# Optimization experiments

Measured on AMD Instinct MI355X. Metric: run time of the kernel, lower is better.

The kernel has to match this reference:

```python
import jax, jax.numpy as jnp
import numpy as np
import math

B, C, H, W = 4, 256, 64, 64
HID = 32  # max(C//8, 32)

def setup_inputs() -> dict:
    key = jax.random.key(0)
    ks = jax.random.split(key, 7)
    x = jax.random.normal(ks[0], (B, C, H, W), dtype=jnp.float32)
    # 1x1 conv weights stored as [out, in]
    w_ce1 = jax.random.normal(ks[1], (HID, C), dtype=jnp.float32) * math.sqrt(2.0 / HID)
    w_ce2 = jax.random.normal(ks[2], (1, HID), dtype=jnp.float32) * math.sqrt(2.0)
    xav = math.sqrt(6.0 / (C + C))
    wq = jax.random.uniform(ks[3], (C, C), jnp.float32, -xav, xav)
    wk = jax.random.uniform(ks[4], (C, C), jnp.float32, -xav, xav)
    wv = jax.random.uniform(ks[5], (C, C), jnp.float32, -xav, xav)
    wproj = jax.random.uniform(ks[6], (C, C), jnp.float32, -xav, xav)
    return {"x": x, "w_ce1": w_ce1, "w_ce2": w_ce2, "wq": wq, "wk": wk, "wv": wv, "wproj": wproj}

def reference(x, w_ce1, w_ce2, wq, wk, wv, wproj):
    b, c, h, w = x.shape
    n = h * w
    # complexity gate: global avg+max pool -> 1x1 convs -> sigmoid, shape [B,1,1,1]
    feat = jnp.mean(x, axis=(2, 3)) + jnp.max(x, axis=(2, 3))       # [B,C]
    hid = jax.nn.silu(jnp.einsum('oc,bc->bo', w_ce1, feat))          # [B,HID]
    complexity = jax.nn.sigmoid(jnp.einsum('oh,bh->bo', w_ce2, hid)) # [B,1]
    complexity = complexity[:, :, None, None]                        # [B,1,1,1]
    # qkv via 1x1 convs, flattened to tokens
    xf = x.reshape(b, c, n)                                          # [B,C,N]
    q = jnp.einsum('oc,bcn->bno', wq, xf)                            # [B,N,C]
    k = jnp.einsum('oc,bcn->bon', wk, xf)                            # [B,C,N]
    v = jnp.einsum('oc,bcn->bno', wv, xf)                            # [B,N,C]
    attn = jax.nn.softmax(jnp.einsum('bnc,bcm->bnm', q, k) * (1.0 / math.sqrt(c)), axis=-1)
    x_attn = jnp.einsum('bnm,bmc->bnc', attn, v)                     # [B,N,C]
    x_attn = x_attn.transpose(0, 2, 1).reshape(b, c, h, w)           # [B,C,H,W]
    proj = jnp.einsum('oc,bchw->bohw', wproj, x_attn)
    return x + proj * complexity
```

## Files before the change

### kernel.cpp

```cpp
#include <hip/hip_runtime.h>
#include <hip/hip_bf16.h>

#define B_ 4
#define C_ 256
#define N_ 4096
#define BN_ (B_*N_)

typedef float f32x4 __attribute__((ext_vector_type(4)));
typedef short bf16x8 __attribute__((ext_vector_type(8)));
typedef short short4v __attribute__((ext_vector_type(4)));

static __device__ __forceinline__ short f2bf(float f){
  unsigned u = __builtin_bit_cast(unsigned, f);
  u += 0x7FFFu + ((u >> 16) & 1u);
  return (short)(u >> 16);
}
static __device__ __forceinline__ float bf2f(short s){
  unsigned u = ((unsigned)(unsigned short)s) << 16;
  return __builtin_bit_cast(float, u);
}
static __device__ __forceinline__ void gload_lds16(const void* g, void* l){
  __builtin_amdgcn_global_load_lds((const __attribute__((address_space(1))) unsigned*)g,
                                   (__attribute__((address_space(3))) unsigned*)l, 16, 0, 0);
}

__global__ __launch_bounds__(256) void k_feat(const float* __restrict__ x, float* __restrict__ feat){
  int row = blockIdx.x;
  const f32x4* p = (const f32x4*)(x + (size_t)row * N_);
  float s = 0.f, mx = -1e30f;
  for (int i = threadIdx.x; i < N_/4; i += 256){
    f32x4 v = p[i];
    s += v.x + v.y + v.z + v.w;
    mx = fmaxf(mx, fmaxf(fmaxf(v.x, v.y), fmaxf(v.z, v.w)));
  }
  __shared__ float ss[256];
  __shared__ float sm[256];
  int t = threadIdx.x;
  ss[t] = s; sm[t] = mx;
  __syncthreads();
  for (int off = 128; off > 0; off >>= 1){
    if (t < off){ ss[t] += ss[t+off]; sm[t] = fmaxf(sm[t], sm[t+off]); }
    __syncthreads();
  }
  if (t == 0) feat[row] = ss[0] * (1.f/(float)N_) + sm[0];
}

__global__ __launch_bounds__(64) void k_cplx(const float* __restrict__ feat, const float* __restrict__ w1,
    const float* __restrict__ w2, float* __restrict__ cplx){
  int b = blockIdx.x, l = threadIdx.x;
  float contrib = 0.f;
  if (l < 32){
    const float* wr = w1 + l*C_;
    const float* f = feat + b*C_;
    float d = 0.f;
    for (int c = 0; c < C_; c++) d += wr[c]*f[c];
    float sg = 1.f/(1.f + expf(-d));
    contrib = (d*sg)*w2[l];
  }
  #pragma unroll
  for (int off = 1; off < 64; off <<= 1) contrib += __shfl_xor(contrib, off);
  if (l == 0) cplx[b] = 1.f/(1.f + expf(-contrib));
}

__global__ __launch_bounds__(256) void k_wcvt(const float* __restrict__ a, const float* __restrict__ b,
    const float* __restrict__ c, const float* __restrict__ d,
    short* __restrict__ oa, short* __restrict__ ob2, short* __restrict__ oc, short* __restrict__ od){
  int m = blockIdx.x >> 6;
  int off = (blockIdx.x & 63)*1024 + threadIdx.x*4;
  const float* src = (m==0)?a:(m==1)?b:(m==2)?c:d;
  short* dst = (m==0)?oa:(m==1)?ob2:(m==2)?oc:od;
  f32x4 v = *(const f32x4*)(src + off);
  short4v s;
  #pragma unroll
  for (int j = 0; j < 4; j++) s[j] = f2bf(v[j]);
  *(short4v*)(dst + off) = s;
}

__global__ __launch_bounds__(256) void k_qkv(const float* __restrict__ x,
    const short* __restrict__ wqb, const short* __restrict__ wkb, const short* __restrict__ wvb,
    short* __restrict__ Q, short* __restrict__ K, short* __restrict__ Vt){
  int b = blockIdx.z, o0 = blockIdx.y*64, n0 = blockIdx.x*64;
  int tid = threadIdx.x, w = tid>>6, l = tid&63, lq = l&15, lg = l>>4;
  const float* xb = x + (size_t)b*C_*N_;
  int nrow = n0 + w*16 + lq;
  f32x4 zero = {0.f,0.f,0.f,0.f};
  f32x4 acc[3][4];
  #pragma unroll
  for (int m = 0; m < 3; m++)
    #pragma unroll
    for (int s = 0; s < 4; s++) acc[m][s] = zero;

  for (int kk = 0; kk < 8; ++kk){
    int c0 = kk*32 + lg*8;
    bf16x8 a;
    #pragma unroll
    for (int j = 0; j < 8; j++) a[j] = f2bf(xb[(size_t)(c0+j)*N_ + nrow]);
    #pragma unroll
    for (int s = 0; s < 4; s++){
      int base = (o0 + s*16 + lq)*C_ + c0;
      bf16x8 aq = *(const bf16x8*)(wqb + base);
      bf16x8 ak = *(const bf16x8*)(wkb + base);
      bf16x8 av = *(const bf16x8*)(wvb + base);
      acc[0][s] = __builtin_amdgcn_mfma_f32_16x16x32_bf16(a, aq, acc[0][s], 0, 0, 0);
      acc[1][s] = __builtin_amdgcn_mfma_f32_16x16x32_bf16(a, ak, acc[1][s], 0, 0, 0);
      acc[2][s] = __builtin_amdgcn_mfma_f32_16x16x32_bf16(a, av, acc[2][s], 0, 0, 0);
    }
  }
  #pragma unroll
  for (int s = 0; s < 4; s++)
    #pragma unroll
    for (int r = 0; r < 4; r++){
      int n = n0 + w*16 + lg*4 + r;
      int o = o0 + s*16 + lq;
      size_t idx = ((size_t)b*N_ + n)*C_ + o;
      Q[idx] = f2bf(acc[0][s][r] * 0.0625f);
      K[idx] = f2bf(acc[1][s][r]);
    }
  __shared__ short lv[64][72];
  #pragma unroll
  for (int s = 0; s < 4; s++)
    #pragma unroll
    for (int r = 0; r < 4; r++)
      lv[s*16 + lq][w*16 + lg*4 + r] = f2bf(acc[2][s][r]);
  __syncthreads();
  #pragma unroll
  for (int i = 0; i < 16; i++){
    int orow = i*4 + (tid>>6);
    int ncol = tid & 63;
    Vt[((size_t)b*C_ + o0 + orow)*N_ + n0 + ncol] = lv[orow][ncol];
  }
}

__global__ __launch_bounds__(512) void k_attn(const short* __restrict__ Q, const short* __restrict__ K,
    const short* __restrict__ Vt, short* __restrict__ Op, float* __restrict__ Mp, float* __restrict__ Lp){
  extern __shared__ short smem[];
  short* Ks = smem;
  short* Vs = smem + 32768;

  int bid = blockIdx.x;
  int xcd = bid & 7;
  int b = xcd >> 1;
  int half = xcd & 1;
  int n0 = (bid >> 3) * 128;
  int kv0 = half * 2048;
  int tid = threadIdx.x, w = tid>>6, l = tid&63, lq = l&15, lg = l>>4;
  const short* Qb = Q + (size_t)b*N_*C_;
  const short* Kb = K + (size_t)b*N_*C_;
  const short* Vb = Vt + (size_t)b*C_*N_;
  short* lp = smem + 65536 + w*(16*72);

  int krow0 = w*8 + (l>>5);
  int kchunk0 = l&31;
  int vrow0 = w*32 + (l>>3);
  int vchunk = (l&7) ^ ((l>>3)&7);

  bf16x8 qf[8];
  {
    const short* qrow = Qb + (size_t)(n0 + w*16 + lq)*C_ + lg*8;
    #pragma unroll
    for (int kk = 0; kk < 8; kk++) qf[kk] = *(const bf16x8*)(qrow + kk*32);
  }
  f32x4 zero = {0.f,0.f,0.f,0.f};
  f32x4 oacc[16];
  #pragma unroll
  for (int c = 0; c < 16; c++) oacc[c] = zero;
  float mrow[4], lsum[4];
  #pragma unroll
  for (int r = 0; r < 4; r++){ mrow[r] = -1e30f; lsum[r] = 0.f; }

  int swz = lq & 7;

  auto stage = [&](int buf, int m0){
    short* kd = Ks + buf*16384 + w*2048;
    short* vd = Vs + buf*16384 + w*2048;
    #pragma unroll
    for (int i = 0; i < 4; i++){
      int row = krow0 + i*2;
      int chunk = kchunk0 ^ (row & 7);
      gload_lds16(Kb + (size_t)(m0 + row)*C_ + chunk*8, kd + i*512);
    }
    #pragma unroll
    for (int i = 0; i < 4; i++){
      int row = vrow0 + i*8;
      gload_lds16(Vb + (size_t)row*N_ + m0 + vchunk*8, vd + i*512);
    }
  };

  stage(0, kv0);
  __syncthreads();
  int cur = 0;

  for (int mt = 0; mt < 32; mt++){
    if (mt + 1 < 32) stage(cur^1, kv0 + (mt+1)*64);

    const short* Kc = Ks + cur*16384;
    const short* Vc = Vs + cur*16384;

    f32x4 sa[4];
    #pragma unroll
    for (int s = 0; s < 4; s++) sa[s] = zero;
    __builtin_amdgcn_s_setprio(1);
    #pragma unroll
    for (int s = 0; s < 4; s++){
      const short* krowp = Kc + (s*16 + lq)*256;
      #pragma unroll
      for (int kk = 0; kk < 8; kk++){
        bf16x8 kf = *(const bf16x8*)(krowp + (((kk*4 + lg) ^ swz) << 3));
        sa[s] = __builtin_amdgcn_mfma_f32_16x16x32_bf16(qf[kk], kf, sa[s], 0, 0, 0);
      }
    }
    __builtin_amdgcn_s_setprio(0);
    float tmax[4];
    #pragma unroll
    for (int r = 0; r < 4; r++){
      float t = fmaxf(fmaxf(sa[0][r], sa[1][r]), fmaxf(sa[2][r], sa[3][r]));
      t = fmaxf(t, __shfl_xor(t, 1));
      t = fmaxf(t, __shfl_xor(t, 2));
      t = fmaxf(t, __shfl_xor(t, 4));
      t = fmaxf(t, __shfl_xor(t, 8));
      tmax[r] = t;
    }
    bool need = (tmax[0] > mrow[0]+8.f) | (tmax[1] > mrow[1]+8.f) |
                (tmax[2] > mrow[2]+8.f) | (tmax[3] > mrow[3]+8.f);
    if (__any(need)){
      float al[4];
      #pragma unroll
      for (int r = 0; r < 4; r++){
        float mn = fmaxf(mrow[r], tmax[r]);
        al[r] = __expf(mrow[r] - mn);
        mrow[r] = mn;
        lsum[r] *= al[r];
      }
      #pragma unroll
      for (int c = 0; c < 16; c++){
        f32x4 o = oacc[c];
        o[0]*=al[0]; o[1]*=al[1]; o[2]*=al[2]; o[3]*=al[3];
        oacc[c] = o;
      }
    }
    #pragma unroll
    for (int s = 0; s < 4; s++)
      #pragma unroll
      for (int r = 0; r < 4; r++)
        sa[s][r] = __expf(sa[s][r] - mrow[r]);
    #pragma unroll
    for (int r = 0; r < 4; r++){
      float t = sa[0][r] + sa[1][r] + sa[2][r] + sa[3][r];
      t += __shfl_xor(t, 1); t += __shfl_xor(t, 2);
      t += __shfl_xor(t, 4); t += __shfl_xor(t, 8);
      lsum[r] += t;
    }
    #pragma unroll
    for (int s = 0; s < 4; s++)
      #pragma unroll
      for (int r = 0; r < 4; r++)
        lp[(lg*4 + r)*72 + s*16 + lq] = f2bf(sa[s][r]);
    __builtin_amdgcn_sched_barrier(0);
    __builtin_amdgcn_s_setprio(1);
    #pragma unroll
    for (int s2 = 0; s2 < 2; s2++){
      bf16x8 pa = *(const bf16x8*)(lp + lq*72 + s2*32 + lg*8);
      #pragma unroll
      for (int c = 0; c < 16; c++){
        bf16x8 vbf = *(const bf16x8*)(Vc + (c*16 + lq)*64 + (((s2*4 + lg) ^ swz) << 3));
        oacc[c] = __builtin_amdgcn_mfma_f32_16x16x32_bf16(pa, vbf, oacc[c], 0, 0, 0);
      }
    }
    __builtin_amdgcn_s_setprio(0);
    __builtin_amdgcn_sched_barrier(0);
    __syncthreads();
    cur ^= 1;
  }
  float inv[4];
  #pragma unroll
  for (int r = 0; r < 4; r++) inv[r] = 1.f / lsum[r];
  #pragma unroll
  for (int c = 0; c < 16; c++)
    #pragma unroll
    for (int r = 0; r < 4; r++){
      int n = n0 + w*16 + lg*4 + r;
      Op[((size_t)half*BN_ + (size_t)b*N_ + n)*C_ + c*16 + lq] = f2bf(oacc[c][r]*inv[r]);
    }
  if (lq == 0){
    #pragma unroll
    for (int r = 0; r < 4; r++){
      int n = n0 + w*16 + lg*4 + r;
      Mp[half*BN_ + b*N_ + n] = mrow[r];
      Lp[half*BN_ + b*N_ + n] = lsum[r];
    }
  }
}

__global__ __launch_bounds__(256) void k_comb(const short* __restrict__ Op, const float* __restrict__ Mp,
    const float* __restrict__ Lp, short* __restrict__ Xa){
  int tid = threadIdx.x;
  int rg = blockIdx.x*8 + (tid>>5);
  int cc = (tid&31)*8;
  float m1 = Mp[rg], m2 = Mp[BN_ + rg];
  float l1 = Lp[rg], l2 = Lp[BN_ + rg];
  float m = fmaxf(m1, m2);
  float w1 = l1 * __expf(m1 - m);
  float w2 = l2 * __expf(m2 - m);
  float inv = 1.f/(w1 + w2);
  w1 *= inv; w2 *= inv;
  bf16x8 o1 = *(const bf16x8*)(Op + (size_t)rg*C_ + cc);
  bf16x8 o2 = *(const bf16x8*)(Op + ((size_t)BN_ + rg)*C_ + cc);
  bf16x8 r;
  #pragma unroll
  for (int j = 0; j < 8; j++){
    float f = w1*bf2f(o1[j]) + w2*bf2f(o2[j]);
    r[j] = f2bf(f);
  }
  *(bf16x8*)(Xa + (size_t)rg*C_ + cc) = r;
}

__global__ __launch_bounds__(256) void k_proj(const float* __restrict__ x, const short* __restrict__ wpb,
    const short* __restrict__ Xa, const float* __restrict__ cplx, float* __restrict__ out){
  int b = blockIdx.z, o0 = blockIdx.y*64, n0 = blockIdx.x*64;
  int tid = threadIdx.x, w = tid>>6, l = tid&63, lq = l&15, lg = l>>4;
  f32x4 zero = {0.f,0.f,0.f,0.f};
  f32x4 acc[4];
  #pragma unroll
  for (int s = 0; s < 4; s++) acc[s] = zero;
  int orow = o0 + w*16 + lq;
  for (int kk = 0; kk < 8; kk++){
    int c0 = kk*32 + lg*8;
    bf16x8 aw = *(const bf16x8*)(wpb + orow*C_ + c0);
    #pragma unroll
    for (int s = 0; s < 4; s++){
      bf16x8 xb = *(const bf16x8*)(Xa + ((size_t)b*N_ + n0 + s*16 + lq)*C_ + c0);
      acc[s] = __builtin_amdgcn_mfma_f32_16x16x32_bf16(aw, xb, acc[s], 0, 0, 0);
    }
  }
  float cp = cplx[b];
  #pragma unroll
  for (int s = 0; s < 4; s++)
    #pragma unroll
    for (int r = 0; r < 4; r++){
      int o = o0 + w*16 + lg*4 + r;
      int n = n0 + s*16 + lq;
      size_t idx = ((size_t)b*C_ + o)*N_ + n;
      out[idx] = x[idx] + cp*acc[s][r];
    }
}

extern "C" void kernel_launch(void* const* d_in, const int* in_sizes, int n_in,
                              void* d_out, int out_size, void* d_ws, size_t ws_size,
                              hipStream_t stream){
  const float* x     = (const float*)d_in[0];
  const float* w_ce1 = (const float*)d_in[1];
  const float* w_ce2 = (const float*)d_in[2];
  const float* wq    = (const float*)d_in[3];
  const float* wk    = (const float*)d_in[4];
  const float* wv    = (const float*)d_in[5];
  const float* wproj = (const float*)d_in[6];
  float* out = (float*)d_out;

  const size_t mat = (size_t)B_*N_*C_;
  short* Q   = (short*)d_ws;
  short* K   = Q + mat;
  short* Vt  = K + mat;
  short* Op  = Vt + mat;
  float* Mp  = (float*)(Op + 2*mat);
  float* Lp  = Mp + 2*BN_;
  float* feat= Lp + 2*BN_;
  float* cplx= feat + B_*C_;
  short* wqb = (short*)(cplx + B_);
  short* wkb = wqb + C_*C_;
  short* wvb = wkb + C_*C_;
  short* wpb = wvb + C_*C_;
  short* Xa  = Q;

  const int SMEM_ATTN = (16384*2 + 16384*2 + 8*16*72) * 2;
  hipFuncSetAttribute((const void*)k_attn, hipFuncAttributeMaxDynamicSharedMemorySize, SMEM_ATTN);

  hipLaunchKernelGGL(k_feat, dim3(B_*C_), dim3(256), 0, stream, x, feat);
  hipLaunchKernelGGL(k_cplx, dim3(B_), dim3(64), 0, stream, feat, w_ce1, w_ce2, cplx);
  hipLaunchKernelGGL(k_wcvt, dim3(256), dim3(256), 0, stream, wq, wk, wv, wproj, wqb, wkb, wvb, wpb);
  hipLaunchKernelGGL(k_qkv, dim3(64,4,4), dim3(256), 0, stream, x, wqb, wkb, wvb, Q, K, Vt);
  hipLaunchKernelGGL(k_attn, dim3(256), dim3(512), SMEM_ATTN, stream, Q, K, Vt, Op, Mp, Lp);
  hipLaunchKernelGGL(k_comb, dim3(BN_/8), dim3(256), 0, stream, Op, Mp, Lp, Xa);
  hipLaunchKernelGGL(k_proj, dim3(64,4,4), dim3(256), 0, stream, x, wpb, Xa, cplx, out);
}
```

Before: 209.6 us.

## Split attention KV range into four parts with single-buffered staging

```diff
diff --git a/kernel.cpp b/kernel.cpp
--- a/kernel.cpp
+++ b/kernel.cpp
@@ -131,12 +131,199 @@
   }
 }
 
-__global__ __launch_bounds__(512) void k_attn(const short* __restrict__ Q, const short* __restrict__ K,
+
+__global__ __launch_bounds__(512) void k_attn4(const short* __restrict__ Q, const short* __restrict__ K,
+    const short* __restrict__ Vt, short* __restrict__ Op, float* __restrict__ Mp, float* __restrict__ Lp){
+  extern __shared__ short smem[];
+  short* Ks = smem;
+  short* Vs = smem + 16384;
+  int bid = blockIdx.x;
+  int xcd = bid & 7, idx = bid >> 3;
+  int b = xcd >> 1;
+  int part = ((xcd & 1) << 1) | (idx & 1);
+  int n0 = (idx >> 1) * 128;
+  int kv0 = part * 1024;
+  int tid = threadIdx.x, w = tid>>6, l = tid&63, lq = l&15, lg = l>>4;
+  const short* Qb = Q + (size_t)b*N_*C_;
+  const short* Kb = K + (size_t)b*N_*C_;
+  const short* Vb = Vt + (size_t)b*C_*N_;
+  short* lp = smem + 32768 + w*(16*64);
+
+  int krow0 = w*8 + (l>>5);
+  int kchunk0 = l&31;
+  int vrow0 = w*32 + (l>>3);
+  int vchunk = (l&7) ^ ((l>>3)&7);
+
+  auto stage = [&](int m0){
+    short* kd = Ks + w*2048;
+    short* vd = Vs + w*2048;
+    #pragma unroll
+    for (int i = 0; i < 4; i++){
+      int row = krow0 + i*2;
+      int chunk = kchunk0 ^ (row & 7);
+      gload_lds16(Kb + (size_t)(m0 + row)*C_ + chunk*8, kd + i*512);
+    }
+    #pragma unroll
+    for (int i = 0; i < 4; i++){
+      int row = vrow0 + i*8;
+      gload_lds16(Vb + (size_t)row*N_ + m0 + vchunk*8, vd + i*512);
+    }
+  };
+
+  stage(kv0);
+
+  bf16x8 qf[8];
+  {
+    const short* qrow = Qb + (size_t)(n0 + w*16 + lq)*C_ + lg*8;
+    #pragma unroll
+    for (int kk = 0; kk < 8; kk++) qf[kk] = *(const bf16x8*)(qrow + kk*32);
+  }
+  f32x4 zero = {0.f,0.f,0.f,0.f};
+  f32x4 oacc[16];
+  #pragma unroll
+  for (int c = 0; c < 16; c++) oacc[c] = zero;
+  float mrow[4], lsum[4];
+  #pragma unroll
+  for (int r = 0; r < 4; r++){ mrow[r] = -1e30f; lsum[r] = 0.f; }
+
+  int swz = lq & 7;
+  __syncthreads();
+
+  for (int mt = 0; mt < 16; mt++){
+    f32x4 sa[4];
+    #pragma unroll
+    for (int s = 0; s < 4; s++) sa[s] = zero;
+    __builtin_amdgcn_s_setprio(1);
+    #pragma unroll
+    for (int s = 0; s < 4; s++){
+      const short* krowp = Ks + (s*16 + lq)*256;
+      #pragma unroll
+      for (int kk = 0; kk < 8; kk++){
+        bf16x8 kf = *(const bf16x8*)(krowp + (((kk*4 + lg) ^ swz) << 3));
+        sa[s] = __builtin_amdgcn_mfma_f32_16x16x32_bf16(qf[kk], kf, sa[s], 0, 0, 0);
+      }
+    }
+    __builtin_amdgcn_s_setprio(0);
+    float tmax[4];
+    #pragma unroll
+    for (int r = 0; r < 4; r++){
+      float t = fmaxf(fmaxf(sa[0][r], sa[1][r]), fmaxf(sa[2][r], sa[3][r]));
+      t = fmaxf(t, __shfl_xor(t, 1));
+      t = fmaxf(t, __shfl_xor(t, 2));
+      t = fmaxf(t, __shfl_xor(t, 4));
+      t = fmaxf(t, __shfl_xor(t, 8));
+      tmax[r] = t;
+    }
+    bool need = (tmax[0] > mrow[0]+8.f) | (tmax[1] > mrow[1]+8.f) |
+                (tmax[2] > mrow[2]+8.f) | (tmax[3] > mrow[3]+8.f);
+    if (__any(need)){
+      float al[4];
+      #pragma unroll
+      for (int r = 0; r < 4; r++){
+        float mn = fmaxf(mrow[r], tmax[r]);
+        al[r] = __expf(mrow[r] - mn);
+        mrow[r] = mn;
+        lsum[r] *= al[r];
+      }
+      #pragma unroll
+      for (int c = 0; c < 16; c++){
+        f32x4 o = oacc[c];
+        o[0]*=al[0]; o[1]*=al[1]; o[2]*=al[2]; o[3]*=al[3];
+        oacc[c] = o;
+      }
+    }
+    #pragma unroll
+    for (int s = 0; s < 4; s++)
+      #pragma unroll
+      for (int r = 0; r < 4; r++)
+        sa[s][r] = __expf(sa[s][r] - mrow[r]);
+    #pragma unroll
+    for (int r = 0; r < 4; r++){
+      float t = sa[0][r] + sa[1][r] + sa[2][r] + sa[3][r];
+      t += __shfl_xor(t, 1); t += __shfl_xor(t, 2);
+      t += __shfl_xor(t, 4); t += __shfl_xor(t, 8);
+      lsum[r] += t;
+    }
+    #pragma unroll
+    for (int s = 0; s < 4; s++)
+      #pragma unroll
+      for (int r = 0; r < 4; r++){
+        int prow = lg*4 + r;
+        int pcol = s*16 + lq;
+        lp[prow*64 + ((((pcol>>3) ^ (prow&7))<<3) | (pcol&7))] = f2bf(sa[s][r]);
+      }
+    __builtin_amdgcn_sched_barrier(0);
+    __builtin_amdgcn_s_setprio(1);
+    #pragma unroll
+    for (int s2 = 0; s2 < 2; s2++){
+      bf16x8 pa = *(const bf16x8*)(lp + lq*64 + (((s2*4 + lg) ^ (lq&7)) << 3));
+      #pragma unroll
+      for (int c = 0; c < 16; c++){
+        bf16x8 vbf = *(const bf16x8*)(Vs + (c*16 + lq)*64 + (((s2*4 + lg) ^ swz) << 3));
+        oacc[c] = __builtin_amdgcn_mfma_f32_16x16x32_bf16(pa, vbf, oacc[c], 0, 0, 0);
+      }
+    }
+    __builtin_amdgcn_s_setprio(0);
+    __builtin_amdgcn_sched_barrier(0);
+    if (mt + 1 < 16){
+      __syncthreads();
+      stage(kv0 + (mt+1)*64);
+      __syncthreads();
+    }
+  }
+  float inv[4];
+  #pragma unroll
+  for (int r = 0; r < 4; r++) inv[r] = 1.f / lsum[r];
+  #pragma unroll
+  for (int c = 0; c < 16; c++)
+    #pragma unroll
+    for (int r = 0; r < 4; r++){
+      int n = n0 + w*16 + lg*4 + r;
+      Op[((size_t)part*BN_ + (size_t)b*N_ + n)*C_ + c*16 + lq] = f2bf(oacc[c][r]*inv[r]);
+    }
+  if (lq == 0){
+    #pragma unroll
+    for (int r = 0; r < 4; r++){
+      int n = n0 + w*16 + lg*4 + r;
+      Mp[part*BN_ + b*N_ + n] = mrow[r];
+      Lp[part*BN_ + b*N_ + n] = lsum[r];
+    }
+  }
+}
+
+__global__ __launch_bounds__(256) void k_comb4(const short* __restrict__ Op, const float* __restrict__ Mp,
+    const float* __restrict__ Lp, short* __restrict__ Xa){
+  int tid = threadIdx.x;
+  int rg = blockIdx.x*8 + (tid>>5);
+  int cc = (tid&31)*8;
+  float mv[4], lv[4];
+  float m = -1e30f;
+  #pragma unroll
+  for (int p = 0; p < 4; p++){ mv[p] = Mp[p*BN_ + rg]; lv[p] = Lp[p*BN_ + rg]; m = fmaxf(m, mv[p]); }
+  float wgt[4], wsum = 0.f;
+  #pragma unroll
+  for (int p = 0; p < 4; p++){ wgt[p] = lv[p]*__expf(mv[p]-m); wsum += wgt[p]; }
+  float inv = 1.f/wsum;
+  float acc[8];
+  #pragma unroll
+  for (int j = 0; j < 8; j++) acc[j] = 0.f;
+  #pragma unroll
+  for (int p = 0; p < 4; p++){
+    bf16x8 o = *(const bf16x8*)(Op + ((size_t)p*BN_ + rg)*C_ + cc);
+    #pragma unroll
+    for (int j = 0; j < 8; j++) acc[j] += wgt[p]*bf2f(o[j]);
+  }
+  bf16x8 r;
+  #pragma unroll
+  for (int j = 0; j < 8; j++) r[j] = f2bf(acc[j]*inv);
+  *(bf16x8*)(Xa + (size_t)rg*C_ + cc) = r;
+}
+
+__global__ __launch_bounds__(512) void k_attn2(const short* __restrict__ Q, const short* __restrict__ K,
     const short* __restrict__ Vt, short* __restrict__ Op, float* __restrict__ Mp, float* __restrict__ Lp){
   extern __shared__ short smem[];
   short* Ks = smem;
   short* Vs = smem + 32768;
-
   int bid = blockIdx.x;
   int xcd = bid & 7;
   int b = xcd >> 1;
@@ -148,12 +335,10 @@
   const short* Kb = K + (size_t)b*N_*C_;
   const short* Vb = Vt + (size_t)b*C_*N_;
   short* lp = smem + 65536 + w*(16*72);
-
   int krow0 = w*8 + (l>>5);
   int kchunk0 = l&31;
   int vrow0 = w*32 + (l>>3);
   int vchunk = (l&7) ^ ((l>>3)&7);
-
   bf16x8 qf[8];
   {
     const short* qrow = Qb + (size_t)(n0 + w*16 + lq)*C_ + lg*8;
@@ -167,9 +352,7 @@
   float mrow[4], lsum[4];
   #pragma unroll
   for (int r = 0; r < 4; r++){ mrow[r] = -1e30f; lsum[r] = 0.f; }
-
   int swz = lq & 7;
-
   auto stage = [&](int buf, int m0){
     short* kd = Ks + buf*16384 + w*2048;
     short* vd = Vs + buf*16384 + w*2048;
@@ -185,17 +368,13 @@
       gload_lds16(Vb + (size_t)row*N_ + m0 + vchunk*8, vd + i*512);
     }
   };
-
   stage(0, kv0);
   __syncthreads();
   int cur = 0;
-
   for (int mt = 0; mt < 32; mt++){
     if (mt + 1 < 32) stage(cur^1, kv0 + (mt+1)*64);
-
     const short* Kc = Ks + cur*16384;
     const short* Vc = Vs + cur*16384;
-
     f32x4 sa[4];
     #pragma unroll
     for (int s = 0; s < 4; s++) sa[s] = zero;
@@ -291,7 +470,7 @@
   }
 }
 
-__global__ __launch_bounds__(256) void k_comb(const short* __restrict__ Op, const float* __restrict__ Mp,
+__global__ __launch_bounds__(256) void k_comb2(const short* __restrict__ Op, const float* __restrict__ Mp,
     const float* __restrict__ Lp, short* __restrict__ Xa){
   int tid = threadIdx.x;
   int rg = blockIdx.x*8 + (tid>>5);
@@ -357,28 +536,40 @@
   float* out = (float*)d_out;
 
   const size_t mat = (size_t)B_*N_*C_;
-  short* Q   = (short*)d_ws;
-  short* K   = Q + mat;
-  short* Vt  = K + mat;
-  short* Op  = Vt + mat;
-  float* Mp  = (float*)(Op + 2*mat);
-  float* Lp  = Mp + 2*BN_;
-  float* feat= Lp + 2*BN_;
-  float* cplx= feat + B_*C_;
-  short* wqb = (short*)(cplx + B_);
-  short* wkb = wqb + C_*C_;
-  short* wvb = wkb + C_*C_;
-  short* wpb = wvb + C_*C_;
+  const size_t needA = (3*mat + 4*mat + 4*(size_t)C_*C_)*2 + (8*(size_t)BN_ + B_*C_ + 16)*4;
+  bool use4 = ws_size >= needA;
+  int nparts = use4 ? 4 : 2;
+
+  char* p = (char*)d_ws;
+  short* Q   = (short*)p;            p += mat*2;
+  short* K   = (short*)p;            p += mat*2;
+  short* Vt  = (short*)p;            p += mat*2;
+  short* Op  = (short*)p;            p += (size_t)nparts*mat*2;
+  float* Mp  = (float*)p;            p += (size_t)nparts*BN_*4;
+  float* Lp  = (float*)p;            p += (size_t)nparts*BN_*4;
+  float* feat= (float*)p;            p += B_*C_*4;
+  float* cplx= (float*)p;            p += 64;
+  short* wqb = (short*)p;            p += (size_t)C_*C_*2;
+  short* wkb = (short*)p;            p += (size_t)C_*C_*2;
+  short* wvb = (short*)p;            p += (size_t)C_*C_*2;
+  short* wpb = (short*)p;
   short* Xa  = Q;
 
-  const int SMEM_ATTN = (16384*2 + 16384*2 + 8*16*72) * 2;
-  hipFuncSetAttribute((const void*)k_attn, hipFuncAttributeMaxDynamicSharedMemorySize, SMEM_ATTN);
+  const int SMEM_A4 = 81920;
+  const int SMEM_A2 = (16384*2 + 16384*2 + 8*16*72) * 2;
+  hipFuncSetAttribute((const void*)k_attn4, hipFuncAttributeMaxDynamicSharedMemorySize, SMEM_A4);
+  hipFuncSetAttribute((const void*)k_attn2, hipFuncAttributeMaxDynamicSharedMemorySize, SMEM_A2);
 
   hipLaunchKernelGGL(k_feat, dim3(B_*C_), dim3(256), 0, stream, x, feat);
   hipLaunchKernelGGL(k_cplx, dim3(B_), dim3(64), 0, stream, feat, w_ce1, w_ce2, cplx);
   hipLaunchKernelGGL(k_wcvt, dim3(256), dim3(256), 0, stream, wq, wk, wv, wproj, wqb, wkb, wvb, wpb);
   hipLaunchKernelGGL(k_qkv, dim3(64,4,4), dim3(256), 0, stream, x, wqb, wkb, wvb, Q, K, Vt);
-  hipLaunchKernelGGL(k_attn, dim3(256), dim3(512), SMEM_ATTN, stream, Q, K, Vt, Op, Mp, Lp);
-  hipLaunchKernelGGL(k_comb, dim3(BN_/8), dim3(256), 0, stream, Op, Mp, Lp, Xa);
+  if (use4){
+    hipLaunchKernelGGL(k_attn4, dim3(512), dim3(512), SMEM_A4, stream, Q, K, Vt, Op, Mp, Lp);
+    hipLaunchKernelGGL(k_comb4, dim3(BN_/8), dim3(256), 0, stream, Op, Mp, Lp, Xa);
+  } else {
+    hipLaunchKernelGGL(k_attn2, dim3(256), dim3(512), SMEM_A2, stream, Q, K, Vt, Op, Mp, Lp);
+    hipLaunchKernelGGL(k_comb2, dim3(BN_/8), dim3(256), 0, stream, Op, Mp, Lp, Xa);
+  }
   hipLaunchKernelGGL(k_proj, dim3(64,4,4), dim3(256), 0, stream, x, wpb, Xa, cplx, out);
 }
```

After: 228.4 us. 9.0% more time.
